# Optimization experiments

Measured on AMD Instinct MI355X. Metric: run time of the kernel, lower is better.

Reference implementation:

```python
import jax, jax.numpy as jnp
import numpy as np

B, C, N, D, H, NC = 128, 9, 2048, 192, 384, 18  # batch, in_chans, time, embed, mlp_hidden, classes


def setup_inputs() -> dict:
    key = jax.random.key(0)
    ks = jax.random.split(key, 18)
    rn = lambda k, sh, s=0.02: jax.random.normal(k, sh, dtype=jnp.float32) * s
    return {
        "x": jax.random.normal(ks[0], (B, C, N), dtype=jnp.float32),
        "conv_w": rn(ks[1], (D, C, 3)),
        "conv_b": jnp.zeros((D,), jnp.float32),
        "pos_embed": jnp.zeros((1, N, D), jnp.float32),
        "qkv_w": rn(ks[2], (3 * D, D)),
        "qkv_b": jnp.zeros((3 * D,), jnp.float32),
        "proj_w": rn(ks[3], (D, D)),
        "proj_b": jnp.zeros((D,), jnp.float32),
        "ln1_g": jnp.ones((D,), jnp.float32),
        "ln1_b": jnp.zeros((D,), jnp.float32),
        "mlp_w1": rn(ks[4], (H, D)),
        "mlp_b1": jnp.zeros((H,), jnp.float32),
        "mlp_w2": rn(ks[5], (D, H)),
        "mlp_b2": jnp.zeros((D,), jnp.float32),
        "ln2_g": jnp.ones((D,), jnp.float32),
        "ln2_b": jnp.zeros((D,), jnp.float32),
        "head_w": rn(ks[6], (NC, D)),
        "head_b": jnp.zeros((NC,), jnp.float32),
    }


def _ln(x, g, b, eps=1e-5):
    m = x.mean(-1, keepdims=True)
    v = ((x - m) ** 2).mean(-1, keepdims=True)
    return (x - m) * jax.lax.rsqrt(v + eps) * g + b


def reference(x, conv_w, conv_b, pos_embed, qkv_w, qkv_b, proj_w, proj_b,
              ln1_g, ln1_b, mlp_w1, mlp_b1, mlp_w2, mlp_b2, ln2_g, ln2_b,
              head_w, head_b):
    # patch embed: Conv1d(C->D, k=3, pad=1), then [B, N, D]
    h = jax.lax.conv_general_dilated(
        x, conv_w, window_strides=(1,), padding=[(1, 1)],
        dimension_numbers=("NCH", "OIH", "NCH")) + conv_b[None, :, None]
    h = jnp.transpose(h, (0, 2, 1)) + pos_embed  # [B, N, D]

    # linear (Performer-style) attention with ReLU feature maps
    hn = _ln(h, ln1_g, ln1_b)
    qkv = hn @ qkv_w.T + qkv_b  # [B, N, 3D]
    q, k, v = jnp.split(qkv, 3, axis=-1)
    q = jax.nn.relu(q)
    k = jax.nn.relu(k)
    kv = jnp.einsum("bnd,bne->bde", k, v)       # [B, D, D]
    num = jnp.einsum("bnd,bde->bne", q, kv)      # [B, N, D]
    # NOTE: original sums q over BOTH token and feature dims -> scalar per batch
    denom = q.sum(axis=(1, 2))[:, None, None]
    attn = num / (denom + 1e-6)
    h = h + attn @ proj_w.T + proj_b

    # MLP block (exact GELU, as torch nn.GELU default)
    hn2 = _ln(h, ln2_g, ln2_b)
    m = jax.nn.gelu(hn2 @ mlp_w1.T + mlp_b1, approximate=False)
    h = h + m @ mlp_w2.T + mlp_b2

    # head: AdaptiveAvgPool1d(1) over time, then Linear
    pooled = h.mean(axis=1)  # [B, D]
    return pooled @ head_w.T + head_b  # [B, NC]
```

## Files before the change

kernel.cpp:

```cpp
#include <hip/hip_runtime.h>
#include <cmath>

#define B_   128
#define C_   9
#define N_   2048
#define D_   192
#define H_   384
#define NC_  18

typedef unsigned short ushort_t;
typedef __attribute__((ext_vector_type(8))) __bf16 bf16x8;
typedef __attribute__((ext_vector_type(8))) short short8;
typedef __attribute__((ext_vector_type(16))) float f32x16;

__device__ __forceinline__ ushort_t f2bf(float x) {
    unsigned u = __float_as_uint(x);
    return (ushort_t)((u + 0x7fffu + ((u >> 16) & 1u)) >> 16);
}
__device__ __forceinline__ float bf2f(ushort_t h) {
    return __uint_as_float(((unsigned)h) << 16);
}
__device__ __forceinline__ bf16x8 ldfrag(const ushort_t* p) {
    short8 s = *(const short8*)p;
    return __builtin_bit_cast(bf16x8, s);
}

__global__ __launch_bounds__(192) void conv_ln_k(
    const float* __restrict__ x, const float* __restrict__ w,
    const float* __restrict__ cb, const float* __restrict__ pos,
    const float* __restrict__ lng, const float* __restrict__ lnb,
    float* __restrict__ h, ushort_t* __restrict__ oh, ushort_t* __restrict__ ol)
{
    const int n0 = blockIdx.x * 64;
    const int b  = blockIdx.y;
    const int d  = threadIdx.x;

    __shared__ float xs[C_][66];
    __shared__ float tile[64][193];
    __shared__ float ps[64][3], pq[64][3];
    __shared__ float mm[64], rr[64];

    for (int e = threadIdx.x; e < C_ * 66; e += 192) {
        int c = e / 66, i = e % 66;
        int n = n0 - 1 + i;
        xs[c][i] = (n >= 0 && n < N_) ? x[((size_t)b * C_ + c) * N_ + n] : 0.f;
    }
    float wr[C_][3];
#pragma unroll
    for (int c = 0; c < C_; ++c)
#pragma unroll
        for (int t = 0; t < 3; ++t) wr[c][t] = w[(d * C_ + c) * 3 + t];
    const float bias = cb[d];
    __syncthreads();

    for (int i = 0; i < 64; ++i) {
        float acc = bias + pos[(size_t)(n0 + i) * D_ + d];
#pragma unroll
        for (int c = 0; c < C_; ++c)
#pragma unroll
            for (int t = 0; t < 3; ++t) acc += xs[c][i + t] * wr[c][t];
        tile[i][d] = acc;
    }
    __syncthreads();

    {
        int row = threadIdx.x & 63, part = threadIdx.x >> 6;
        float s = 0.f, q = 0.f;
        const float* tr = &tile[row][part * 64];
#pragma unroll 8
        for (int j = 0; j < 64; ++j) { float v = tr[j]; s += v; q += v * v; }
        ps[row][part] = s; pq[row][part] = q;
    }
    __syncthreads();
    if (threadIdx.x < 64) {
        int r = threadIdx.x;
        float s = ps[r][0] + ps[r][1] + ps[r][2];
        float q = pq[r][0] + pq[r][1] + pq[r][2];
        float m = s * (1.f / D_);
        mm[r] = m;
        rr[r] = rsqrtf(q * (1.f / D_) - m * m + 1e-5f);
    }
    __syncthreads();
    {
        const float gd = lng[d], bd = lnb[d];
        for (int i = 0; i < 64; ++i) {
            float v = tile[i][d];
            size_t idx = ((size_t)b * N_ + n0 + i) * D_ + d;
            h[idx] = v;
            float nv = (v - mm[i]) * rr[i] * gd + bd;
            ushort_t hb = f2bf(nv);
            oh[idx] = hb;
            ol[idx] = f2bf(nv - bf2f(hb));
        }
    }
}

__global__ __launch_bounds__(256) void splitw_pack_k(
    const float* __restrict__ w, ushort_t* __restrict__ hi, ushort_t* __restrict__ lo,
    int NW, int K)
{
    int i = blockIdx.x * 256 + threadIdx.x;
    if (i >= NW * K) return;
    int row = i / K, k = i % K;
    int g = row / 192, c = row % 192;
    float v = w[i];
    ushort_t hb = f2bf(v);
    size_t o = (size_t)g * K * 192 + (size_t)(k >> 4) * 3072 + (size_t)c * 16 + (k & 15);
    hi[o] = hb;
    lo[o] = f2bf(v - bf2f(hb));
}

template <int EPI, int KT, int NBY>
__global__ __launch_bounds__(256) void mgemm(
    const ushort_t* __restrict__ Ah, const ushort_t* __restrict__ Al,
    const ushort_t* __restrict__ Wh, const ushort_t* __restrict__ Wl,
    const float* __restrict__ bias, float* __restrict__ dsum,
    const float* __restrict__ lng, const float* __restrict__ lnb,
    ushort_t* __restrict__ oh, ushort_t* __restrict__ ol,
    ushort_t* __restrict__ kTh, ushort_t* __restrict__ kTl,
    ushort_t* __restrict__ vTh, ushort_t* __restrict__ vTl,
    float* __restrict__ facc)
{
    extern __shared__ ushort_t smem[];
    constexpr int NS  = KT / 16;
    constexpr int APL = 12288;

    const int tid  = threadIdx.x;
    const int lane = tid & 63;
    const int l5   = lane >> 5;
    const int wid  = tid >> 6;
    const int wr = wid >> 1, wc = wid & 1;

    int bx, by;
    {
        int gmx = gridDim.x / NBY;
        int xx = blockIdx.x & 7, ii = blockIdx.x >> 3;
        by = ii % NBY;
        bx = xx * (gmx >> 3) + ii / NBY;
    }
    const int m0 = bx * 64;
    const int batch = m0 >> 11;

    size_t wbase = 0;
    if (EPI == 0) wbase = (size_t)by * 192 * KT;
    else if (EPI == 3) wbase = (size_t)batch * D_ * D_;
    const ushort_t* Whp = Wh + wbase;
    const ushort_t* Wlp = Wl + wbase;

    auto stageChunk = [&](int kr) {
#pragma unroll
        for (int i = 0; i < 12; ++i) {
            int c = wid + i * 4;
            int plane = c & 1, k8 = c >> 1;
            const ushort_t* ap = plane ? Al : Ah;
            const ushort_t* src = ap + (size_t)(m0 + lane) * KT + kr * 192 + k8 * 8;
            __builtin_amdgcn_global_load_lds(
                (const __attribute__((address_space(1))) void*)src,
                (__attribute__((address_space(3))) void*)(smem + plane * APL + k8 * 512),
                16, 0, 0);
        }
    };

    const int wcol = (wc * 96 + (lane & 31)) * 16 + l5 * 8;
    auto loadW = [&](int sg, bf16x8* w) {
#pragma unroll
        for (int tn = 0; tn < 3; ++tn) {
            size_t off = (size_t)sg * 3072 + wcol + tn * 512;
            w[tn * 2 + 0] = ldfrag(Whp + off);
            w[tn * 2 + 1] = ldfrag(Wlp + off);
        }
    };

    f32x16 acc[3] = {};
    const int arow = (wr * 32 + (lane & 31)) * 8;

    bf16x8 w0[6], w1[6], w2[6];
    loadW(0, w0);
    if (NS > 1) loadW(1, w1);
    if (NS > 2) loadW(2, w2);

#pragma unroll
    for (int s = 0; s < NS; ++s) {
        if ((s % 12) == 0) {
            if (s) __syncthreads();
            stageChunk(s / 12);
            __syncthreads();
        }
        bf16x8* wcur = (s % 3 == 0) ? w0 : ((s % 3 == 1) ? w1 : w2);
        int ao = ((s % 12) * 2 + l5) * 512 + arow;
        bf16x8 ah = ldfrag(smem + ao);
        bf16x8 al = ldfrag(smem + APL + ao);
#pragma unroll
        for (int tn = 0; tn < 3; ++tn) {
            acc[tn] = __builtin_amdgcn_mfma_f32_32x32x16_bf16(ah, wcur[tn * 2 + 0], acc[tn], 0, 0, 0);
            acc[tn] = __builtin_amdgcn_mfma_f32_32x32x16_bf16(ah, wcur[tn * 2 + 1], acc[tn], 0, 0, 0);
            acc[tn] = __builtin_amdgcn_mfma_f32_32x32x16_bf16(al, wcur[tn * 2 + 0], acc[tn], 0, 0, 0);
        }
        if (s + 3 < NS) loadW(s + 3, wcur);
    }

    const int cb = wc * 96 + (lane & 31);
    const int rb0 = m0 + wr * 32 + 4 * l5;
    const int rl0 = wr * 32 + 4 * l5;

    if (EPI == 0) {
        if (by == 0) {
            float qsum = 0.f;
            __syncthreads();
#pragma unroll
            for (int tn = 0; tn < 3; ++tn) {
                const int col = cb + tn * 32;
                const float bv = bias[col];
#pragma unroll
                for (int r = 0; r < 16; ++r) {
                    int rowl = rl0 + (r & 3) + 8 * (r >> 2);
                    float v = fmaxf(acc[tn][r] + bv, 0.f);
                    qsum += v;
                    ushort_t hb = f2bf(v);
                    smem[rowl * 192 + col] = hb;
                    smem[APL + rowl * 192 + col] = f2bf(v - bf2f(hb));
                }
            }
            __syncthreads();
            {
                size_t gb = (size_t)m0 * 192;
#pragma unroll
                for (int j = 0; j < 6; ++j) {
                    int idx = (tid * 6 + j) * 8;
                    *(uint4*)(oh + gb + idx) = *(const uint4*)&smem[idx];
                    *(uint4*)(ol + gb + idx) = *(const uint4*)&smem[APL + idx];
                }
            }
            float* red = (float*)(smem + 2 * APL);
            red[tid] = qsum;
            __syncthreads();
            for (int o = 128; o > 0; o >>= 1) {
                if (tid < o) red[tid] += red[tid + o];
                __syncthreads();
            }
            if (tid == 0) dsum[batch * 32 + ((m0 >> 6) & 31)] = red[0];
        } else {
            ushort_t* dsth = (by == 1) ? kTh : vTh;
            ushort_t* dstl = (by == 1) ? kTl : vTl;
            constexpr int STR = 72;
#pragma unroll
            for (int plane = 0; plane < 2; ++plane) {
                __syncthreads();
#pragma unroll
                for (int tn = 0; tn < 3; ++tn) {
                    const int col = cb + tn * 32;
                    const float bv = bias[by * 192 + col];
#pragma unroll
                    for (int r = 0; r < 16; ++r) {
                        int rowl = rl0 + (r & 3) + 8 * (r >> 2);
                        float v = acc[tn][r] + bv;
                        if (by == 1) v = fmaxf(v, 0.f);
                        ushort_t hb = f2bf(v);
                        smem[col * STR + rowl] = plane ? f2bf(v - bf2f(hb)) : hb;
                    }
                }
                __syncthreads();
                if (tid < 192) {
                    ushort_t* dst = plane ? dstl : dsth;
                    size_t gbase = ((size_t)batch * 192 + tid) * (size_t)N_ + (m0 & 2047);
#pragma unroll
                    for (int i2 = 0; i2 < 8; ++i2)
                        *(uint4*)(dst + gbase + i2 * 8) = *(const uint4*)&smem[tid * STR + i2 * 8];
                }
            }
        }
    } else if (EPI == 3) {
        float ds = 0.f;
        const float* dp = dsum + batch * 32;
#pragma unroll
        for (int j = 0; j < 32; ++j) ds += dp[j];
        const float s = 1.f / (ds + 1e-6f);
#pragma unroll
        for (int tn = 0; tn < 3; ++tn) {
            const int col = cb + tn * 32;
            const float bv = bias[col];
#pragma unroll
            for (int r = 0; r < 16; ++r) {
                int row = rb0 + (r & 3) + 8 * (r >> 2);
                float v = facc[(size_t)row * D_ + col] + acc[tn][r] * s + bv;
                facc[(size_t)row * D_ + col] = v;
                acc[tn][r] = v;
            }
        }
        __syncthreads();
        float* ls = (float*)(smem + 2 * APL);
        float* lq = ls + 128;
        float* lm = lq + 128;
        float* lr = lm + 64;
#pragma unroll
        for (int r = 0; r < 16; ++r) {
            float pv = acc[0][r] + acc[1][r] + acc[2][r];
            float qv = acc[0][r] * acc[0][r] + acc[1][r] * acc[1][r] + acc[2][r] * acc[2][r];
#pragma unroll
            for (int off = 1; off <= 16; off <<= 1) {
                pv += __shfl_xor(pv, off);
                qv += __shfl_xor(qv, off);
            }
            if ((lane & 31) == 0) {
                int rl = rl0 + (r & 3) + 8 * (r >> 2);
                ls[rl * 2 + wc] = pv;
                lq[rl * 2 + wc] = qv;
            }
        }
        __syncthreads();
        if (tid < 64) {
            float sv = ls[tid * 2] + ls[tid * 2 + 1];
            float qv = lq[tid * 2] + lq[tid * 2 + 1];
            float mv = sv * (1.f / D_);
            lm[tid] = mv;
            lr[tid] = rsqrtf(qv * (1.f / D_) - mv * mv + 1e-5f);
        }
        __syncthreads();
#pragma unroll
        for (int tn = 0; tn < 3; ++tn) {
            const int col = cb + tn * 32;
            const float gv = lng[col], bv2 = lnb[col];
#pragma unroll
            for (int r = 0; r < 16; ++r) {
                int rl = rl0 + (r & 3) + 8 * (r >> 2);
                float nv = (acc[tn][r] - lm[rl]) * lr[rl] * gv + bv2;
                ushort_t hb = f2bf(nv);
                smem[rl * 192 + col] = hb;
                smem[APL + rl * 192 + col] = f2bf(nv - bf2f(hb));
            }
        }
        __syncthreads();
        {
            size_t gb = (size_t)m0 * 192;
#pragma unroll
            for (int j = 0; j < 6; ++j) {
                int idx = (tid * 6 + j) * 8;
                *(uint4*)(oh + gb + idx) = *(const uint4*)&smem[idx];
                *(uint4*)(ol + gb + idx) = *(const uint4*)&smem[APL + idx];
            }
        }
    }
}

__global__ __launch_bounds__(256) void fused_mlp(
    const ushort_t* __restrict__ Ah, const ushort_t* __restrict__ Al,
    const ushort_t* __restrict__ W1h, const ushort_t* __restrict__ W1l,
    const ushort_t* __restrict__ W2h, const ushort_t* __restrict__ W2l,
    const float* __restrict__ b1, const float* __restrict__ b2,
    float* __restrict__ h, float* __restrict__ pooled)
{
    extern __shared__ ushort_t smem[];
    constexpr int APL = 12288;

    const int tid  = threadIdx.x;
    const int lane = tid & 63;
    const int l5   = lane >> 5;
    const int wid  = tid >> 6;
    const int wr = wid >> 1, wc = wid & 1;

    int bx;
    { int xx = blockIdx.x & 7, ii = blockIdx.x >> 3; bx = xx * (gridDim.x >> 3) + ii; }
    const int m0 = bx * 64;
    const int batch = m0 >> 11;

#pragma unroll
    for (int i = 0; i < 12; ++i) {
        int c = wid + i * 4;
        int plane = c & 1, k8 = c >> 1;
        const ushort_t* ap = plane ? Al : Ah;
        const ushort_t* src = ap + (size_t)(m0 + lane) * 192 + k8 * 8;
        __builtin_amdgcn_global_load_lds(
            (const __attribute__((address_space(1))) void*)src,
            (__attribute__((address_space(3))) void*)(smem + plane * APL + k8 * 512),
            16, 0, 0);
    }
    __syncthreads();

    const int wcol = (wc * 96 + (lane & 31)) * 16 + l5 * 8;
    const int arow = (wr * 32 + (lane & 31)) * 8;

    auto loadWf = [&](const ushort_t* Wh, const ushort_t* Wl, int sg, bf16x8* w) {
#pragma unroll
        for (int tn = 0; tn < 3; ++tn) {
            size_t off = (size_t)sg * 3072 + wcol + tn * 512;
            w[tn * 2 + 0] = ldfrag(Wh + off);
            w[tn * 2 + 1] = ldfrag(Wl + off);
        }
    };

    f32x16 accm[2][3] = {};
#pragma unroll
    for (int g = 0; g < 2; ++g) {
        const ushort_t* Wh = W1h + g * 36864;
        const ushort_t* Wl = W1l + g * 36864;
        bf16x8 w0[6], w1[6], w2[6];
        loadWf(Wh, Wl, 0, w0);
        loadWf(Wh, Wl, 1, w1);
        loadWf(Wh, Wl, 2, w2);
#pragma unroll
        for (int s = 0; s < 12; ++s) {
            bf16x8* wcur = (s % 3 == 0) ? w0 : ((s % 3 == 1) ? w1 : w2);
            int ao = (s * 2 + l5) * 512 + arow;
            bf16x8 ah = ldfrag(smem + ao);
            bf16x8 al = ldfrag(smem + APL + ao);
#pragma unroll
            for (int tn = 0; tn < 3; ++tn) {
                accm[g][tn] = __builtin_amdgcn_mfma_f32_32x32x16_bf16(ah, wcur[tn * 2 + 0], accm[g][tn], 0, 0, 0);
                accm[g][tn] = __builtin_amdgcn_mfma_f32_32x32x16_bf16(ah, wcur[tn * 2 + 1], accm[g][tn], 0, 0, 0);
                accm[g][tn] = __builtin_amdgcn_mfma_f32_32x32x16_bf16(al, wcur[tn * 2 + 0], accm[g][tn], 0, 0, 0);
            }
            if (s + 3 < 12) loadWf(Wh, Wl, s + 3, wcur);
        }
    }

    f32x16 acco[3] = {};
#pragma unroll
    for (int g = 0; g < 2; ++g) {
        __syncthreads();
#pragma unroll
        for (int tn = 0; tn < 3; ++tn) {
            const int cl = wc * 96 + tn * 32 + (lane & 31);
            const float bv = b1[g * 192 + cl];
#pragma unroll
            for (int r = 0; r < 16; ++r) {
                int rowl = wr * 32 + 4 * l5 + (r & 3) + 8 * (r >> 2);
                float v = accm[g][tn][r] + bv;
                float gv = 0.5f * v * (1.f + erff(v * 0.70710678118654752f));
                ushort_t hb = f2bf(gv);
                int ad = ((cl >> 3) * 64 + rowl) * 8 + (cl & 7);
                smem[ad] = hb;
                smem[APL + ad] = f2bf(gv - bf2f(hb));
            }
        }
        __syncthreads();
        bf16x8 w0[6], w1[6], w2[6];
        loadWf(W2h, W2l, g * 12 + 0, w0);
        loadWf(W2h, W2l, g * 12 + 1, w1);
        loadWf(W2h, W2l, g * 12 + 2, w2);
#pragma unroll
        for (int s = 0; s < 12; ++s) {
            bf16x8* wcur = (s % 3 == 0) ? w0 : ((s % 3 == 1) ? w1 : w2);
            int ao = (s * 2 + l5) * 512 + arow;
            bf16x8 ah = ldfrag(smem + ao);
            bf16x8 al = ldfrag(smem + APL + ao);
#pragma unroll
            for (int tn = 0; tn < 3; ++tn) {
                acco[tn] = __builtin_amdgcn_mfma_f32_32x32x16_bf16(ah, wcur[tn * 2 + 0], acco[tn], 0, 0, 0);
                acco[tn] = __builtin_amdgcn_mfma_f32_32x32x16_bf16(ah, wcur[tn * 2 + 1], acco[tn], 0, 0, 0);
                acco[tn] = __builtin_amdgcn_mfma_f32_32x32x16_bf16(al, wcur[tn * 2 + 0], acco[tn], 0, 0, 0);
            }
            if (s + 3 < 12) loadWf(W2h, W2l, g * 12 + s + 3, wcur);
        }
    }

    const int cb = wc * 96 + (lane & 31);
    const int rb0 = m0 + wr * 32 + 4 * l5;
    float tsum[3] = {0.f, 0.f, 0.f};
#pragma unroll
    for (int tn = 0; tn < 3; ++tn) {
        const int col = cb + tn * 32;
        const float bv = b2[col];
#pragma unroll
        for (int r = 0; r < 16; ++r) {
            int row = rb0 + (r & 3) + 8 * (r >> 2);
            float v = h[(size_t)row * D_ + col] + acco[tn][r] + bv;
            h[(size_t)row * D_ + col] = v;
            tsum[tn] += v;
        }
    }
#pragma unroll
    for (int tn = 0; tn < 3; ++tn) {
        float t = tsum[tn];
        t += __shfl_xor(t, 32);
        if (l5 == 0) atomicAdd(&pooled[(size_t)batch * D_ + cb + tn * 32], t);
    }
}

__global__ __launch_bounds__(256) void mgemm_kv(
    const ushort_t* __restrict__ Ah, const ushort_t* __restrict__ Al,
    const ushort_t* __restrict__ Wh, const ushort_t* __restrict__ Wl,
    float* __restrict__ facc, size_t span)
{
    extern __shared__ ushort_t smem[];
    constexpr int BM = 64;
    constexpr int APL = BM * 32, AK = BM * 8, AELEMS = BM * 64;
    constexpr int BUFE = AELEMS + 12288;
    constexpr int ACH = 8, NCH = ACH + 24;

    const int tid  = threadIdx.x;
    const int lane = tid & 63;
    const int l5   = lane >> 5;
    const int wid  = tid >> 6;
    const int wr = wid >> 1, wc = wid & 1;
    const int bx = blockIdx.x;
    const int m0 = bx * BM;

    const size_t wbase = (size_t)(bx / 3) * 192 * (size_t)N_;
    const ushort_t* Whp = Wh + wbase;
    const ushort_t* Wlp = Wl + wbase;

    const int seg = N_ / gridDim.z;
    const int kbeg = blockIdx.z * seg, kend = kbeg + seg;

    auto stage = [&](int buf, int k0) {
        const int base = buf * BUFE;
#pragma unroll
        for (int i = 0; i < NCH / 4; ++i) {
            int c = wid + i * 4;
            const ushort_t* src;
            int dst;
            if (c < ACH) {
                int koct = c & 3, tt = c >> 2;
                int plane = tt & 1;
                const ushort_t* ap = plane ? Al : Ah;
                src = ap + (size_t)(m0 + lane) * N_ + k0 + koct * 8;
                dst = plane * APL + koct * AK;
            } else {
                int c2 = c - ACH;
                int koct = c2 & 3, tt = c2 >> 2;
                int plane = tt & 1, rb = tt >> 1;
                const ushort_t* wp = plane ? Wlp : Whp;
                src = wp + (size_t)(rb * 64 + lane) * N_ + k0 + koct * 8;
                dst = AELEMS + plane * 6144 + koct * 1536 + rb * 512;
            }
            __builtin_amdgcn_global_load_lds(
                (const __attribute__((address_space(1))) void*)src,
                (__attribute__((address_space(3))) void*)(smem + base + dst),
                16, 0, 0);
        }
    };

    f32x16 acc[3] = {};

    const int nt = (kend - kbeg) / 32;
    stage(0, kbeg);
    __syncthreads();
    int cur = 0;
    for (int t = 0; t < nt; ++t) {
        if (t + 1 < nt) stage(cur ^ 1, kbeg + (t + 1) * 32);
        const ushort_t* bb = smem + cur * BUFE;
#pragma unroll
        for (int kh = 0; kh < 2; ++kh) {
            int ao = (kh * 2 + l5) * AK + (wr * 32 + (lane & 31)) * 8;
            bf16x8 ah = ldfrag(bb + ao);
            bf16x8 al = ldfrag(bb + APL + ao);
#pragma unroll
            for (int tn = 0; tn < 3; ++tn) {
                int wo = AELEMS + (kh * 2 + l5) * 1536 + (wc * 96 + tn * 32 + (lane & 31)) * 8;
                bf16x8 wh = ldfrag(bb + wo);
                bf16x8 wl = ldfrag(bb + wo + 6144);
                acc[tn] = __builtin_amdgcn_mfma_f32_32x32x16_bf16(ah, wh, acc[tn], 0, 0, 0);
                acc[tn] = __builtin_amdgcn_mfma_f32_32x32x16_bf16(ah, wl, acc[tn], 0, 0, 0);
                acc[tn] = __builtin_amdgcn_mfma_f32_32x32x16_bf16(al, wh, acc[tn], 0, 0, 0);
            }
        }
        __syncthreads();
        cur ^= 1;
    }

    float* fz = facc + (size_t)blockIdx.z * span;
    const int cb = wc * 96 + (lane & 31);
    const int rb0 = m0 + wr * 32 + 4 * l5;
#pragma unroll
    for (int tn = 0; tn < 3; ++tn) {
        const int col = cb + tn * 32;
#pragma unroll
        for (int r = 0; r < 16; ++r) {
            int row = rb0 + (r & 3) + 8 * (r >> 2);
            fz[(size_t)row * D_ + col] = acc[tn][r];
        }
    }
}

__global__ __launch_bounds__(256) void kv2_k(
    const float* __restrict__ pw, const float* __restrict__ kvs, size_t span,
    ushort_t* __restrict__ oh, ushort_t* __restrict__ ol)
{
    __shared__ float As[16][68];
    __shared__ float Ws[16][68];
    const int tid = threadIdx.x;
    const int tx = tid & 15, ty = tid >> 4;
    const int m0 = blockIdx.x * 64;
    const int n0 = blockIdx.y * 64;
    const int b = blockIdx.z;
    const int lm = tid >> 2;
    const int lk = (tid & 3) * 4;

    float acc[4][4] = {};
    for (int k0 = 0; k0 < D_; k0 += 16) {
        float4 av = *(const float4*)(pw + (size_t)(m0 + lm) * D_ + k0 + lk);
        As[lk + 0][lm] = av.x; As[lk + 1][lm] = av.y;
        As[lk + 2][lm] = av.z; As[lk + 3][lm] = av.w;
        const float* base = kvs + (size_t)b * D_ * D_ + (size_t)(n0 + lm) * D_ + k0 + lk;
        float4 wv = {0.f, 0.f, 0.f, 0.f};
#pragma unroll
        for (int z = 0; z < 8; ++z) {
            float4 t = *(const float4*)(base + z * span);
            wv.x += t.x; wv.y += t.y; wv.z += t.z; wv.w += t.w;
        }
        Ws[lk + 0][lm] = wv.x; Ws[lk + 1][lm] = wv.y;
        Ws[lk + 2][lm] = wv.z; Ws[lk + 3][lm] = wv.w;
        __syncthreads();
#pragma unroll
        for (int kk = 0; kk < 16; ++kk) {
            float4 a4 = *(const float4*)&As[kk][ty * 4];
            float4 w4 = *(const float4*)&Ws[kk][tx * 4];
            float a[4] = {a4.x, a4.y, a4.z, a4.w};
            float w[4] = {w4.x, w4.y, w4.z, w4.w};
#pragma unroll
            for (int i = 0; i < 4; ++i)
#pragma unroll
                for (int j = 0; j < 4; ++j) acc[i][j] += a[i] * w[j];
        }
        __syncthreads();
    }
    const int d0 = n0 + tx * 4;
#pragma unroll
    for (int i = 0; i < 4; ++i) {
        ushort_t hb[4], lb[4];
#pragma unroll
        for (int j = 0; j < 4; ++j) {
            float v = acc[i][j];
            hb[j] = f2bf(v);
            lb[j] = f2bf(v - bf2f(hb[j]));
        }
        const int e = m0 + ty * 4 + i;
        size_t off = (size_t)b * D_ * D_ + ((size_t)(d0 >> 4) * 192 + e) * 16 + (d0 & 15);
        *(uint2*)&oh[off] = make_uint2((unsigned)hb[0] | ((unsigned)hb[1] << 16),
                                       (unsigned)hb[2] | ((unsigned)hb[3] << 16));
        *(uint2*)&ol[off] = make_uint2((unsigned)lb[0] | ((unsigned)lb[1] << 16),
                                       (unsigned)lb[2] | ((unsigned)lb[3] << 16));
    }
}

__global__ __launch_bounds__(192) void head_k(
    const float* __restrict__ pooled, const float* __restrict__ hw,
    const float* __restrict__ hb, float* __restrict__ out)
{
    const int b = blockIdx.x, d = threadIdx.x;
    __shared__ float p[D_];
    p[d] = pooled[(size_t)b * D_ + d] * (1.f / N_);
    __syncthreads();
    if (d < NC_) {
        float acc = hb[d];
        for (int e = 0; e < D_; ++e) acc += p[e] * hw[d * D_ + e];
        out[b * NC_ + d] = acc;
    }
}

extern "C" void kernel_launch(void* const* d_in, const int* in_sizes, int n_in,
                              void* d_out, int out_size, void* d_ws, size_t ws_size,
                              hipStream_t stream) {
    (void)in_sizes; (void)n_in; (void)out_size;

    const float* x      = (const float*)d_in[0];
    const float* conv_w = (const float*)d_in[1];
    const float* conv_b = (const float*)d_in[2];
    const float* pos    = (const float*)d_in[3];
    const float* qkv_w  = (const float*)d_in[4];
    const float* qkv_b  = (const float*)d_in[5];
    const float* proj_w = (const float*)d_in[6];
    const float* proj_b = (const float*)d_in[7];
    const float* ln1_g  = (const float*)d_in[8];
    const float* ln1_b  = (const float*)d_in[9];
    const float* mlp_w1 = (const float*)d_in[10];
    const float* mlp_b1 = (const float*)d_in[11];
    const float* mlp_w2 = (const float*)d_in[12];
    const float* mlp_b2 = (const float*)d_in[13];
    const float* ln2_g  = (const float*)d_in[14];
    const float* ln2_b  = (const float*)d_in[15];
    const float* head_w = (const float*)d_in[16];
    const float* head_b = (const float*)d_in[17];
    float* out = (float*)d_out;

    const size_t perB =
        (size_t)N_ * D_ * 4 +
        (size_t)N_ * D_ * 2 * 2 +
        (size_t)N_ * D_ * 2 * 2 +
        (size_t)N_ * D_ * 2 * 4 +
        (size_t)D_ * D_ * 2 * 2 +
        16384;
    const size_t fixedW = 2ull * (576 * 192 + 384 * 192 + 192 * 384) * 2 + 65536;
    int BC = B_;
    while (BC > 1 && fixedW + (size_t)BC * perB > ws_size) BC >>= 1;
    const int nchunks = B_ / BC;
    const size_t rows = (size_t)BC * N_;

    char* p = (char*)d_ws;
    auto alloc = [&](size_t bytes) -> char* {
        char* r = p;
        p += (bytes + 255) & ~(size_t)255;
        return r;
    };
    ushort_t* qw_hi = (ushort_t*)alloc(576 * 192 * 2);
    ushort_t* qw_lo = (ushort_t*)alloc(576 * 192 * 2);
    ushort_t* w1_hi = (ushort_t*)alloc(384 * 192 * 2);
    ushort_t* w1_lo = (ushort_t*)alloc(384 * 192 * 2);
    ushort_t* w2_hi = (ushort_t*)alloc(192 * 384 * 2);
    ushort_t* w2_lo = (ushort_t*)alloc(192 * 384 * 2);

    const size_t szPl = rows * D_ * 2;
    float*    h      = (float*)alloc(rows * D_ * 4);
    ushort_t* hn_hi  = (ushort_t*)alloc(szPl);
    ushort_t* hn_lo  = (ushort_t*)alloc(szPl);
    ushort_t* q_hi   = (ushort_t*)alloc(szPl);
    ushort_t* q_lo   = (ushort_t*)alloc(szPl);
    ushort_t* kT_hi  = (ushort_t*)alloc(szPl);
    ushort_t* kT_lo  = (ushort_t*)alloc(szPl);
    ushort_t* vT_hi  = (ushort_t*)alloc(szPl);
    ushort_t* vT_lo  = (ushort_t*)alloc(szPl);
    ushort_t* kv2t_h = (ushort_t*)alloc((size_t)BC * D_ * D_ * 2);
    ushort_t* kv2t_l = (ushort_t*)alloc((size_t)BC * D_ * D_ * 2);
    float*    dsum   = (float*)alloc((size_t)BC * 32 * 4);
    float*    pooled = (float*)alloc((size_t)BC * D_ * 4);
    float*    kvs    = (float*)hn_hi;
    const size_t kvspan = (size_t)BC * D_ * D_;

    splitw_pack_k<<<(576 * 192 + 255) / 256, 256, 0, stream>>>(qkv_w, qw_hi, qw_lo, 576, 192);
    splitw_pack_k<<<(384 * 192 + 255) / 256, 256, 0, stream>>>(mlp_w1, w1_hi, w1_lo, 384, 192);
    splitw_pack_k<<<(192 * 384 + 255) / 256, 256, 0, stream>>>(mlp_w2, w2_hi, w2_lo, 192, 384);

    const int gm = (int)(rows / 64);
    const size_t SHL = 50688;
    const size_t SHM = 49152;
    const size_t SH4 = (size_t)(64 * 64 + 12288) * 2 * 2;

    for (int ch = 0; ch < nchunks; ++ch) {
        const int b0 = ch * BC;
        const float* xc = x + (size_t)b0 * C_ * N_;

        hipMemsetAsync(pooled, 0, (size_t)BC * D_ * 4, stream);

        conv_ln_k<<<dim3(N_ / 64, BC), 192, 0, stream>>>(
            xc, conv_w, conv_b, pos, ln1_g, ln1_b, h, hn_hi, hn_lo);
        mgemm<0, 192, 3><<<gm * 3, 256, SHL, stream>>>(
            hn_hi, hn_lo, qw_hi, qw_lo, qkv_b, dsum, nullptr, nullptr,
            q_hi, q_lo, kT_hi, kT_lo, vT_hi, vT_lo, nullptr);
        mgemm_kv<<<dim3(BC * 3, 1, 8), 256, SH4, stream>>>(
            kT_hi, kT_lo, vT_hi, vT_lo, kvs, kvspan);
        kv2_k<<<dim3(3, 3, BC), 256, 0, stream>>>(proj_w, kvs, kvspan, kv2t_h, kv2t_l);
        mgemm<3, 192, 1><<<gm, 256, SHL, stream>>>(
            q_hi, q_lo, kv2t_h, kv2t_l, proj_b, dsum, ln2_g, ln2_b,
            hn_hi, hn_lo, nullptr, nullptr, nullptr, nullptr, h);
        fused_mlp<<<gm, 256, SHM, stream>>>(
            hn_hi, hn_lo, w1_hi, w1_lo, w2_hi, w2_lo, mlp_b1, mlp_b2, h, pooled);
        head_k<<<BC, 192, 0, stream>>>(pooled, head_w, head_b, out + (size_t)b0 * NC_);
    }
}
```

Measured before the change: 1.557 ms.

## Fuse attention projection, LayerNorm2 and MLP into one kernel with padded LDS

Merges the attention-output GEMM (q·kv2 plus residual and LN2) with the fused MLP kernel, so the LN2 output stays in shared memory instead of being written to and re-read from global hn buffers. The final residual h is no longer written back; only the pooled sum is accumulated, since h is used nowhere else. The A-tile LDS layout gains padding (a stride of 520 instead of 512) to reduce bank conflicts. The qkv GEMM is specialised into its own kernel. Costs are higher register pressure and more LDS in the fused kernel.

```diff
diff --git a/kernel.cpp b/kernel.cpp
--- a/kernel.cpp
+++ b/kernel.cpp
@@ -24,6 +24,8 @@
     short8 s = *(const short8*)p;
     return __builtin_bit_cast(bf16x8, s);
 }
+
+#define APAD 12480
 
 __global__ __launch_bounds__(192) void conv_ln_k(
     const float* __restrict__ x, const float* __restrict__ w,
@@ -110,19 +112,15 @@
     lo[o] = f2bf(v - bf2f(hb));
 }
 
-template <int EPI, int KT, int NBY>
-__global__ __launch_bounds__(256) void mgemm(
+__global__ __launch_bounds__(256) void qkv_k(
     const ushort_t* __restrict__ Ah, const ushort_t* __restrict__ Al,
     const ushort_t* __restrict__ Wh, const ushort_t* __restrict__ Wl,
     const float* __restrict__ bias, float* __restrict__ dsum,
-    const float* __restrict__ lng, const float* __restrict__ lnb,
     ushort_t* __restrict__ oh, ushort_t* __restrict__ ol,
     ushort_t* __restrict__ kTh, ushort_t* __restrict__ kTl,
-    ushort_t* __restrict__ vTh, ushort_t* __restrict__ vTl,
-    float* __restrict__ facc)
+    ushort_t* __restrict__ vTh, ushort_t* __restrict__ vTl)
 {
     extern __shared__ ushort_t smem[];
-    constexpr int NS  = KT / 16;
     constexpr int APL = 12288;
 
     const int tid  = threadIdx.x;
@@ -133,235 +131,16 @@
 
     int bx, by;
     {
-        int gmx = gridDim.x / NBY;
+        int gmx = gridDim.x / 3;
         int xx = blockIdx.x & 7, ii = blockIdx.x >> 3;
-        by = ii % NBY;
-        bx = xx * (gmx >> 3) + ii / NBY;
+        by = ii % 3;
+        bx = xx * (gmx >> 3) + ii / 3;
     }
     const int m0 = bx * 64;
     const int batch = m0 >> 11;
 
-    size_t wbase = 0;
-    if (EPI == 0) wbase = (size_t)by * 192 * KT;
-    else if (EPI == 3) wbase = (size_t)batch * D_ * D_;
-    const ushort_t* Whp = Wh + wbase;
-    const ushort_t* Wlp = Wl + wbase;
-
-    auto stageChunk = [&](int kr) {
-#pragma unroll
-        for (int i = 0; i < 12; ++i) {
-            int c = wid + i * 4;
-            int plane = c & 1, k8 = c >> 1;
-            const ushort_t* ap = plane ? Al : Ah;
-            const ushort_t* src = ap + (size_t)(m0 + lane) * KT + kr * 192 + k8 * 8;
-            __builtin_amdgcn_global_load_lds(
-                (const __attribute__((address_space(1))) void*)src,
-                (__attribute__((address_space(3))) void*)(smem + plane * APL + k8 * 512),
-                16, 0, 0);
-        }
-    };
-
-    const int wcol = (wc * 96 + (lane & 31)) * 16 + l5 * 8;
-    auto loadW = [&](int sg, bf16x8* w) {
-#pragma unroll
-        for (int tn = 0; tn < 3; ++tn) {
-            size_t off = (size_t)sg * 3072 + wcol + tn * 512;
-            w[tn * 2 + 0] = ldfrag(Whp + off);
-            w[tn * 2 + 1] = ldfrag(Wlp + off);
-        }
-    };
-
-    f32x16 acc[3] = {};
-    const int arow = (wr * 32 + (lane & 31)) * 8;
-
-    bf16x8 w0[6], w1[6], w2[6];
-    loadW(0, w0);
-    if (NS > 1) loadW(1, w1);
-    if (NS > 2) loadW(2, w2);
-
-#pragma unroll
-    for (int s = 0; s < NS; ++s) {
-        if ((s % 12) == 0) {
-            if (s) __syncthreads();
-            stageChunk(s / 12);
-            __syncthreads();
-        }
-        bf16x8* wcur = (s % 3 == 0) ? w0 : ((s % 3 == 1) ? w1 : w2);
-        int ao = ((s % 12) * 2 + l5) * 512 + arow;
-        bf16x8 ah = ldfrag(smem + ao);
-        bf16x8 al = ldfrag(smem + APL + ao);
-#pragma unroll
-        for (int tn = 0; tn < 3; ++tn) {
-            acc[tn] = __builtin_amdgcn_mfma_f32_32x32x16_bf16(ah, wcur[tn * 2 + 0], acc[tn], 0, 0, 0);
-            acc[tn] = __builtin_amdgcn_mfma_f32_32x32x16_bf16(ah, wcur[tn * 2 + 1], acc[tn], 0, 0, 0);
-            acc[tn] = __builtin_amdgcn_mfma_f32_32x32x16_bf16(al, wcur[tn * 2 + 0], acc[tn], 0, 0, 0);
-        }
-        if (s + 3 < NS) loadW(s + 3, wcur);
-    }
-
-    const int cb = wc * 96 + (lane & 31);
-    const int rb0 = m0 + wr * 32 + 4 * l5;
-    const int rl0 = wr * 32 + 4 * l5;
-
-    if (EPI == 0) {
-        if (by == 0) {
-            float qsum = 0.f;
-            __syncthreads();
-#pragma unroll
-            for (int tn = 0; tn < 3; ++tn) {
-                const int col = cb + tn * 32;
-                const float bv = bias[col];
-#pragma unroll
-                for (int r = 0; r < 16; ++r) {
-                    int rowl = rl0 + (r & 3) + 8 * (r >> 2);
-                    float v = fmaxf(acc[tn][r] + bv, 0.f);
-                    qsum += v;
-                    ushort_t hb = f2bf(v);
-                    smem[rowl * 192 + col] = hb;
-                    smem[APL + rowl * 192 + col] = f2bf(v - bf2f(hb));
-                }
-            }
-            __syncthreads();
-            {
-                size_t gb = (size_t)m0 * 192;
-#pragma unroll
-                for (int j = 0; j < 6; ++j) {
-                    int idx = (tid * 6 + j) * 8;
-                    *(uint4*)(oh + gb + idx) = *(const uint4*)&smem[idx];
-                    *(uint4*)(ol + gb + idx) = *(const uint4*)&smem[APL + idx];
-                }
-            }
-            float* red = (float*)(smem + 2 * APL);
-            red[tid] = qsum;
-            __syncthreads();
-            for (int o = 128; o > 0; o >>= 1) {
-                if (tid < o) red[tid] += red[tid + o];
-                __syncthreads();
-            }
-            if (tid == 0) dsum[batch * 32 + ((m0 >> 6) & 31)] = red[0];
-        } else {
-            ushort_t* dsth = (by == 1) ? kTh : vTh;
-            ushort_t* dstl = (by == 1) ? kTl : vTl;
-            constexpr int STR = 72;
-#pragma unroll
-            for (int plane = 0; plane < 2; ++plane) {
-                __syncthreads();
-#pragma unroll
-                for (int tn = 0; tn < 3; ++tn) {
-                    const int col = cb + tn * 32;
-                    const float bv = bias[by * 192 + col];
-#pragma unroll
-                    for (int r = 0; r < 16; ++r) {
-                        int rowl = rl0 + (r & 3) + 8 * (r >> 2);
-                        float v = acc[tn][r] + bv;
-                        if (by == 1) v = fmaxf(v, 0.f);
-                        ushort_t hb = f2bf(v);
-                        smem[col * STR + rowl] = plane ? f2bf(v - bf2f(hb)) : hb;
-                    }
-                }
-                __syncthreads();
-                if (tid < 192) {
-                    ushort_t* dst = plane ? dstl : dsth;
-                    size_t gbase = ((size_t)batch * 192 + tid) * (size_t)N_ + (m0 & 2047);
-#pragma unroll
-                    for (int i2 = 0; i2 < 8; ++i2)
-                        *(uint4*)(dst + gbase + i2 * 8) = *(const uint4*)&smem[tid * STR + i2 * 8];
-                }
-            }
-        }
-    } else if (EPI == 3) {
-        float ds = 0.f;
-        const float* dp = dsum + batch * 32;
-#pragma unroll
-        for (int j = 0; j < 32; ++j) ds += dp[j];
-        const float s = 1.f / (ds + 1e-6f);
-#pragma unroll
-        for (int tn = 0; tn < 3; ++tn) {
-            const int col = cb + tn * 32;
-            const float bv = bias[col];
-#pragma unroll
-            for (int r = 0; r < 16; ++r) {
-                int row = rb0 + (r & 3) + 8 * (r >> 2);
-                float v = facc[(size_t)row * D_ + col] + acc[tn][r] * s + bv;
-                facc[(size_t)row * D_ + col] = v;
-                acc[tn][r] = v;
-            }
-        }
-        __syncthreads();
-        float* ls = (float*)(smem + 2 * APL);
-        float* lq = ls + 128;
-        float* lm = lq + 128;
-        float* lr = lm + 64;
-#pragma unroll
-        for (int r = 0; r < 16; ++r) {
-            float pv = acc[0][r] + acc[1][r] + acc[2][r];
-            float qv = acc[0][r] * acc[0][r] + acc[1][r] * acc[1][r] + acc[2][r] * acc[2][r];
-#pragma unroll
-            for (int off = 1; off <= 16; off <<= 1) {
-                pv += __shfl_xor(pv, off);
-                qv += __shfl_xor(qv, off);
-            }
-            if ((lane & 31) == 0) {
-                int rl = rl0 + (r & 3) + 8 * (r >> 2);
-                ls[rl * 2 + wc] = pv;
-                lq[rl * 2 + wc] = qv;
-            }
-        }
-        __syncthreads();
-        if (tid < 64) {
-            float sv = ls[tid * 2] + ls[tid * 2 + 1];
-            float qv = lq[tid * 2] + lq[tid * 2 + 1];
-            float mv = sv * (1.f / D_);
-            lm[tid] = mv;
-            lr[tid] = rsqrtf(qv * (1.f / D_) - mv * mv + 1e-5f);
-        }
-        __syncthreads();
-#pragma unroll
-        for (int tn = 0; tn < 3; ++tn) {
-            const int col = cb + tn * 32;
-            const float gv = lng[col], bv2 = lnb[col];
-#pragma unroll
-            for (int r = 0; r < 16; ++r) {
-                int rl = rl0 + (r & 3) + 8 * (r >> 2);
-                float nv = (acc[tn][r] - lm[rl]) * lr[rl] * gv + bv2;
-                ushort_t hb = f2bf(nv);
-                smem[rl * 192 + col] = hb;
-                smem[APL + rl * 192 + col] = f2bf(nv - bf2f(hb));
-            }
-        }
-        __syncthreads();
-        {
-            size_t gb = (size_t)m0 * 192;
-#pragma unroll
-            for (int j = 0; j < 6; ++j) {
-                int idx = (tid * 6 + j) * 8;
-                *(uint4*)(oh + gb + idx) = *(const uint4*)&smem[idx];
-                *(uint4*)(ol + gb + idx) = *(const uint4*)&smem[APL + idx];
-            }
-        }
-    }
-}
-
-__global__ __launch_bounds__(256) void fused_mlp(
-    const ushort_t* __restrict__ Ah, const ushort_t* __restrict__ Al,
-    const ushort_t* __restrict__ W1h, const ushort_t* __restrict__ W1l,
-    const ushort_t* __restrict__ W2h, const ushort_t* __restrict__ W2l,
-    const float* __restrict__ b1, const float* __restrict__ b2,
-    float* __restrict__ h, float* __restrict__ pooled)
-{
-    extern __shared__ ushort_t smem[];
-    constexpr int APL = 12288;
-
-    const int tid  = threadIdx.x;
-    const int lane = tid & 63;
-    const int l5   = lane >> 5;
-    const int wid  = tid >> 6;
-    const int wr = wid >> 1, wc = wid & 1;
-
-    int bx;
-    { int xx = blockIdx.x & 7, ii = blockIdx.x >> 3; bx = xx * (gridDim.x >> 3) + ii; }
-    const int m0 = bx * 64;
-    const int batch = m0 >> 11;
+    const ushort_t* Whp = Wh + (size_t)by * 192 * 192;
+    const ushort_t* Wlp = Wl + (size_t)by * 192 * 192;
 
 #pragma unroll
     for (int i = 0; i < 12; ++i) {
@@ -378,7 +157,142 @@
 
     const int wcol = (wc * 96 + (lane & 31)) * 16 + l5 * 8;
     const int arow = (wr * 32 + (lane & 31)) * 8;
-
+    auto loadW = [&](int sg, bf16x8* w) {
+#pragma unroll
+        for (int tn = 0; tn < 3; ++tn) {
+            size_t off = (size_t)sg * 3072 + wcol + tn * 512;
+            w[tn * 2 + 0] = ldfrag(Whp + off);
+            w[tn * 2 + 1] = ldfrag(Wlp + off);
+        }
+    };
+
+    f32x16 acc[3] = {};
+    bf16x8 w0[6], w1[6], w2[6];
+    loadW(0, w0); loadW(1, w1); loadW(2, w2);
+
+#pragma unroll
+    for (int s = 0; s < 12; ++s) {
+        bf16x8* wcur = (s % 3 == 0) ? w0 : ((s % 3 == 1) ? w1 : w2);
+        int ao = (s * 2 + l5) * 512 + arow;
+        bf16x8 ah = ldfrag(smem + ao);
+        bf16x8 al = ldfrag(smem + APL + ao);
+#pragma unroll
+        for (int tn = 0; tn < 3; ++tn) {
+            acc[tn] = __builtin_amdgcn_mfma_f32_32x32x16_bf16(ah, wcur[tn * 2 + 0], acc[tn], 0, 0, 0);
+            acc[tn] = __builtin_amdgcn_mfma_f32_32x32x16_bf16(ah, wcur[tn * 2 + 1], acc[tn], 0, 0, 0);
+            acc[tn] = __builtin_amdgcn_mfma_f32_32x32x16_bf16(al, wcur[tn * 2 + 0], acc[tn], 0, 0, 0);
+        }
+        if (s + 3 < 12) loadW(s + 3, wcur);
+    }
+
+    const int cb = wc * 96 + (lane & 31);
+    const int rl0 = wr * 32 + 4 * l5;
+
+    if (by == 0) {
+        float qsum = 0.f;
+        __syncthreads();
+#pragma unroll
+        for (int tn = 0; tn < 3; ++tn) {
+            const int col = cb + tn * 32;
+            const float bv = bias[col];
+#pragma unroll
+            for (int r = 0; r < 16; ++r) {
+                int rowl = rl0 + (r & 3) + 8 * (r >> 2);
+                float v = fmaxf(acc[tn][r] + bv, 0.f);
+                qsum += v;
+                ushort_t hb = f2bf(v);
+                smem[rowl * 192 + col] = hb;
+                smem[APL + rowl * 192 + col] = f2bf(v - bf2f(hb));
+            }
+        }
+        __syncthreads();
+        {
+            size_t gb = (size_t)m0 * 192;
+#pragma unroll
+            for (int j = 0; j < 6; ++j) {
+                int idx = (tid * 6 + j) * 8;
+                *(uint4*)(oh + gb + idx) = *(const uint4*)&smem[idx];
+                *(uint4*)(ol + gb + idx) = *(const uint4*)&smem[APL + idx];
+            }
+        }
+        float* red = (float*)(smem + 2 * APL);
+        red[tid] = qsum;
+        __syncthreads();
+        for (int o = 128; o > 0; o >>= 1) {
+            if (tid < o) red[tid] += red[tid + o];
+            __syncthreads();
+        }
+        if (tid == 0) dsum[batch * 32 + ((m0 >> 6) & 31)] = red[0];
+    } else {
+        ushort_t* dsth = (by == 1) ? kTh : vTh;
+        ushort_t* dstl = (by == 1) ? kTl : vTl;
+        constexpr int STR = 72;
+#pragma unroll
+        for (int plane = 0; plane < 2; ++plane) {
+            __syncthreads();
+#pragma unroll
+            for (int tn = 0; tn < 3; ++tn) {
+                const int col = cb + tn * 32;
+                const float bv = bias[by * 192 + col];
+#pragma unroll
+                for (int r = 0; r < 16; ++r) {
+                    int rowl = rl0 + (r & 3) + 8 * (r >> 2);
+                    float v = acc[tn][r] + bv;
+                    if (by == 1) v = fmaxf(v, 0.f);
+                    ushort_t hb = f2bf(v);
+                    smem[col * STR + rowl] = plane ? f2bf(v - bf2f(hb)) : hb;
+                }
+            }
+            __syncthreads();
+            if (tid < 192) {
+                ushort_t* dst = plane ? dstl : dsth;
+                size_t gbase = ((size_t)batch * 192 + tid) * (size_t)N_ + (m0 & 2047);
+#pragma unroll
+                for (int i2 = 0; i2 < 8; ++i2)
+                    *(uint4*)(dst + gbase + i2 * 8) = *(const uint4*)&smem[tid * STR + i2 * 8];
+            }
+        }
+    }
+}
+
+__global__ __launch_bounds__(256) void attn_mlp_k(
+    const ushort_t* __restrict__ qh, const ushort_t* __restrict__ ql,
+    const ushort_t* __restrict__ kv2h, const ushort_t* __restrict__ kv2l,
+    const ushort_t* __restrict__ W1h, const ushort_t* __restrict__ W1l,
+    const ushort_t* __restrict__ W2h, const ushort_t* __restrict__ W2l,
+    const float* __restrict__ projb, const float* __restrict__ dsum,
+    const float* __restrict__ lng, const float* __restrict__ lnb,
+    const float* __restrict__ b1, const float* __restrict__ b2,
+    const float* __restrict__ h, float* __restrict__ pooled)
+{
+    extern __shared__ ushort_t smem[];
+
+    const int tid  = threadIdx.x;
+    const int lane = tid & 63;
+    const int l5   = lane >> 5;
+    const int wid  = tid >> 6;
+    const int wr = wid >> 1, wc = wid & 1;
+
+    int bx;
+    { int xx = blockIdx.x & 7, ii = blockIdx.x >> 3; bx = xx * (gridDim.x >> 3) + ii; }
+    const int m0 = bx * 64;
+    const int batch = m0 >> 11;
+
+#pragma unroll
+    for (int i = 0; i < 12; ++i) {
+        int c = wid + i * 4;
+        int plane = c & 1, kk = c >> 1;
+        const ushort_t* ap = plane ? ql : qh;
+        const ushort_t* src = ap + (size_t)(m0 + lane) * 192 + kk * 8;
+        __builtin_amdgcn_global_load_lds(
+            (const __attribute__((address_space(1))) void*)src,
+            (__attribute__((address_space(3))) void*)(smem + plane * APAD + kk * 520),
+            16, 0, 0);
+    }
+    __syncthreads();
+
+    const int wcol = (wc * 96 + (lane & 31)) * 16 + l5 * 8;
+    const int arow = (wr * 32 + (lane & 31)) * 8;
     auto loadWf = [&](const ushort_t* Wh, const ushort_t* Wl, int sg, bf16x8* w) {
 #pragma unroll
         for (int tn = 0; tn < 3; ++tn) {
@@ -388,21 +302,111 @@
         }
     };
 
+    const ushort_t* AWh = kv2h + (size_t)batch * 36864;
+    const ushort_t* AWl = kv2l + (size_t)batch * 36864;
+    f32x16 acc[3] = {};
+    {
+        bf16x8 w0[6], w1[6], w2[6];
+        loadWf(AWh, AWl, 0, w0); loadWf(AWh, AWl, 1, w1); loadWf(AWh, AWl, 2, w2);
+#pragma unroll
+        for (int s = 0; s < 12; ++s) {
+            bf16x8* wcur = (s % 3 == 0) ? w0 : ((s % 3 == 1) ? w1 : w2);
+            int ao = (s * 2 + l5) * 520 + arow;
+            bf16x8 ah = ldfrag(smem + ao);
+            bf16x8 al = ldfrag(smem + APAD + ao);
+#pragma unroll
+            for (int tn = 0; tn < 3; ++tn) {
+                acc[tn] = __builtin_amdgcn_mfma_f32_32x32x16_bf16(ah, wcur[tn * 2 + 0], acc[tn], 0, 0, 0);
+                acc[tn] = __builtin_amdgcn_mfma_f32_32x32x16_bf16(ah, wcur[tn * 2 + 1], acc[tn], 0, 0, 0);
+                acc[tn] = __builtin_amdgcn_mfma_f32_32x32x16_bf16(al, wcur[tn * 2 + 0], acc[tn], 0, 0, 0);
+            }
+            if (s + 3 < 12) loadWf(AWh, AWl, s + 3, wcur);
+        }
+    }
+
+    const int cb = wc * 96 + (lane & 31);
+    const int rb0 = m0 + wr * 32 + 4 * l5;
+    const int rl0 = wr * 32 + 4 * l5;
+
+    float ds = 0.f;
+    {
+        const float* dp = dsum + batch * 32;
+#pragma unroll
+        for (int j = 0; j < 32; ++j) ds += dp[j];
+    }
+    const float sc = 1.f / (ds + 1e-6f);
+    float tsum[3] = {0.f, 0.f, 0.f};
+#pragma unroll
+    for (int tn = 0; tn < 3; ++tn) {
+        const int col = cb + tn * 32;
+        const float bv = projb[col];
+#pragma unroll
+        for (int r = 0; r < 16; ++r) {
+            int row = rb0 + (r & 3) + 8 * (r >> 2);
+            float v = h[(size_t)row * D_ + col] + acc[tn][r] * sc + bv;
+            acc[tn][r] = v;
+            tsum[tn] += v;
+        }
+    }
+
+    float* ls = (float*)(smem + 2 * APAD);
+    float* lq = ls + 128;
+    float* lm = lq + 128;
+    float* lr = lm + 64;
+#pragma unroll
+    for (int r = 0; r < 16; ++r) {
+        float pv = acc[0][r] + acc[1][r] + acc[2][r];
+        float qv = acc[0][r] * acc[0][r] + acc[1][r] * acc[1][r] + acc[2][r] * acc[2][r];
+#pragma unroll
+        for (int off = 1; off <= 16; off <<= 1) {
+            pv += __shfl_xor(pv, off);
+            qv += __shfl_xor(qv, off);
+        }
+        if ((lane & 31) == 0) {
+            int rl = rl0 + (r & 3) + 8 * (r >> 2);
+            ls[rl * 2 + wc] = pv;
+            lq[rl * 2 + wc] = qv;
+        }
+    }
+    __syncthreads();
+    if (tid < 64) {
+        float sv = ls[tid * 2] + ls[tid * 2 + 1];
+        float qv = lq[tid * 2] + lq[tid * 2 + 1];
+        float mv = sv * (1.f / D_);
+        lm[tid] = mv;
+        lr[tid] = rsqrtf(qv * (1.f / D_) - mv * mv + 1e-5f);
+    }
+    __syncthreads();
+
+#pragma unroll
+    for (int tn = 0; tn < 3; ++tn) {
+        const int col = cb + tn * 32;
+        const float gv = lng[col], bv2 = lnb[col];
+#pragma unroll
+        for (int r = 0; r < 16; ++r) {
+            int rl = rl0 + (r & 3) + 8 * (r >> 2);
+            float nv = (acc[tn][r] - lm[rl]) * lr[rl] * gv + bv2;
+            ushort_t hb = f2bf(nv);
+            int ad = (col >> 3) * 520 + rl * 8 + (col & 7);
+            smem[ad] = hb;
+            smem[APAD + ad] = f2bf(nv - bf2f(hb));
+        }
+    }
+    __syncthreads();
+
     f32x16 accm[2][3] = {};
 #pragma unroll
     for (int g = 0; g < 2; ++g) {
         const ushort_t* Wh = W1h + g * 36864;
         const ushort_t* Wl = W1l + g * 36864;
         bf16x8 w0[6], w1[6], w2[6];
-        loadWf(Wh, Wl, 0, w0);
-        loadWf(Wh, Wl, 1, w1);
-        loadWf(Wh, Wl, 2, w2);
+        loadWf(Wh, Wl, 0, w0); loadWf(Wh, Wl, 1, w1); loadWf(Wh, Wl, 2, w2);
 #pragma unroll
         for (int s = 0; s < 12; ++s) {
             bf16x8* wcur = (s % 3 == 0) ? w0 : ((s % 3 == 1) ? w1 : w2);
-            int ao = (s * 2 + l5) * 512 + arow;
+            int ao = (s * 2 + l5) * 520 + arow;
             bf16x8 ah = ldfrag(smem + ao);
-            bf16x8 al = ldfrag(smem + APL + ao);
+            bf16x8 al = ldfrag(smem + APAD + ao);
 #pragma unroll
             for (int tn = 0; tn < 3; ++tn) {
                 accm[g][tn] = __builtin_amdgcn_mfma_f32_32x32x16_bf16(ah, wcur[tn * 2 + 0], accm[g][tn], 0, 0, 0);
@@ -423,13 +427,13 @@
             const float bv = b1[g * 192 + cl];
 #pragma unroll
             for (int r = 0; r < 16; ++r) {
-                int rowl = wr * 32 + 4 * l5 + (r & 3) + 8 * (r >> 2);
+                int rowl = rl0 + (r & 3) + 8 * (r >> 2);
                 float v = accm[g][tn][r] + bv;
                 float gv = 0.5f * v * (1.f + erff(v * 0.70710678118654752f));
                 ushort_t hb = f2bf(gv);
-                int ad = ((cl >> 3) * 64 + rowl) * 8 + (cl & 7);
+                int ad = (cl >> 3) * 520 + rowl * 8 + (cl & 7);
                 smem[ad] = hb;
-                smem[APL + ad] = f2bf(gv - bf2f(hb));
+                smem[APAD + ad] = f2bf(gv - bf2f(hb));
             }
         }
         __syncthreads();
@@ -440,9 +444,9 @@
 #pragma unroll
         for (int s = 0; s < 12; ++s) {
             bf16x8* wcur = (s % 3 == 0) ? w0 : ((s % 3 == 1) ? w1 : w2);
-            int ao = (s * 2 + l5) * 512 + arow;
+            int ao = (s * 2 + l5) * 520 + arow;
             bf16x8 ah = ldfrag(smem + ao);
-            bf16x8 al = ldfrag(smem + APL + ao);
+            bf16x8 al = ldfrag(smem + APAD + ao);
 #pragma unroll
             for (int tn = 0; tn < 3; ++tn) {
                 acco[tn] = __builtin_amdgcn_mfma_f32_32x32x16_bf16(ah, wcur[tn * 2 + 0], acco[tn], 0, 0, 0);
@@ -453,26 +457,14 @@
         }
     }
 
-    const int cb = wc * 96 + (lane & 31);
-    const int rb0 = m0 + wr * 32 + 4 * l5;
-    float tsum[3] = {0.f, 0.f, 0.f};
 #pragma unroll
     for (int tn = 0; tn < 3; ++tn) {
         const int col = cb + tn * 32;
-        const float bv = b2[col];
-#pragma unroll
-        for (int r = 0; r < 16; ++r) {
-            int row = rb0 + (r & 3) + 8 * (r >> 2);
-            float v = h[(size_t)row * D_ + col] + acco[tn][r] + bv;
-            h[(size_t)row * D_ + col] = v;
-            tsum[tn] += v;
-        }
-    }
-#pragma unroll
-    for (int tn = 0; tn < 3; ++tn) {
-        float t = tsum[tn];
+        float t = tsum[tn] + 16.f * b2[col];
+#pragma unroll
+        for (int r = 0; r < 16; ++r) t += acco[tn][r];
         t += __shfl_xor(t, 32);
-        if (l5 == 0) atomicAdd(&pooled[(size_t)batch * D_ + cb + tn * 32], t);
+        if (l5 == 0) atomicAdd(&pooled[(size_t)batch * D_ + col], t);
     }
 }
 
@@ -721,8 +713,8 @@
     splitw_pack_k<<<(192 * 384 + 255) / 256, 256, 0, stream>>>(mlp_w2, w2_hi, w2_lo, 192, 384);
 
     const int gm = (int)(rows / 64);
-    const size_t SHL = 50688;
-    const size_t SHM = 49152;
+    const size_t SHQ = 50688;
+    const size_t SHM = (size_t)APAD * 2 * 2 + 1536;
     const size_t SH4 = (size_t)(64 * 64 + 12288) * 2 * 2;
 
     for (int ch = 0; ch < nchunks; ++ch) {
@@ -733,17 +725,15 @@
 
         conv_ln_k<<<dim3(N_ / 64, BC), 192, 0, stream>>>(
             xc, conv_w, conv_b, pos, ln1_g, ln1_b, h, hn_hi, hn_lo);
-        mgemm<0, 192, 3><<<gm * 3, 256, SHL, stream>>>(
-            hn_hi, hn_lo, qw_hi, qw_lo, qkv_b, dsum, nullptr, nullptr,
-            q_hi, q_lo, kT_hi, kT_lo, vT_hi, vT_lo, nullptr);
+        qkv_k<<<gm * 3, 256, SHQ, stream>>>(
+            hn_hi, hn_lo, qw_hi, qw_lo, qkv_b, dsum,
+            q_hi, q_lo, kT_hi, kT_lo, vT_hi, vT_lo);
         mgemm_kv<<<dim3(BC * 3, 1, 8), 256, SH4, stream>>>(
             kT_hi, kT_lo, vT_hi, vT_lo, kvs, kvspan);
         kv2_k<<<dim3(3, 3, BC), 256, 0, stream>>>(proj_w, kvs, kvspan, kv2t_h, kv2t_l);
-        mgemm<3, 192, 1><<<gm, 256, SHL, stream>>>(
-            q_hi, q_lo, kv2t_h, kv2t_l, proj_b, dsum, ln2_g, ln2_b,
-            hn_hi, hn_lo, nullptr, nullptr, nullptr, nullptr, h);
-        fused_mlp<<<gm, 256, SHM, stream>>>(
-            hn_hi, hn_lo, w1_hi, w1_lo, w2_hi, w2_lo, mlp_b1, mlp_b2, h, pooled);
+        attn_mlp_k<<<gm, 256, SHM, stream>>>(
+            q_hi, q_lo, kv2t_h, kv2t_l, w1_hi, w1_lo, w2_hi, w2_lo,
+            proj_b, dsum, ln2_g, ln2_b, mlp_b1, mlp_b2, h, pooled);
         head_k<<<BC, 192, 0, stream>>>(pooled, head_w, head_b, out + (size_t)b0 * NC_);
     }
 }
```

After: 1.704 ms. 9.5% more time.
